# Kernel tuning notes

Measured on AMD Instinct MI355X. Metric: run time of the kernel, lower is better.

The kernel has to match this reference:

```python
import jax, jax.numpy as jnp
import numpy as np

V = 96103   # pegasus-xsum vocab
D = 1024    # d_model
H = 16      # heads
DH = D // H
F = 4096    # ffn
L = 2       # enc and dec layers (reduced from 16 for the reference)
S = 512     # source length
T = 80      # max_length
B = 4       # batch of sources
NS = 5      # num_return_sequences
BN = B * NS # decode streams
TOPK = 100
EOS = 1
MINLEN = 7
EMB_SCALE = float(np.sqrt(D))


def ln(x):
    m = jnp.mean(x, -1, keepdims=True)
    v = jnp.mean((x - m) ** 2, -1, keepdims=True)
    return (x - m) * jax.lax.rsqrt(v + 1e-5)


def setup_inputs() -> dict:
    key = jax.random.key(0)
    ks = jax.random.split(key, 16)
    g = lambda k, s: (jax.random.normal(k, s) * 0.02).astype(jnp.float32)
    return {
        "ids": jax.random.randint(ks[0], (B, S), 0, 96000).astype(jnp.int32),
        "mask": jnp.ones((B, S), jnp.int32),
        "E": g(ks[1], (V, D)),
        "pos_e": g(ks[2], (S, D)),
        "pos_d": g(ks[3], (T, D)),
        "enc_attn_in": g(ks[4], (L, D, 3 * D)),
        "enc_attn_out": g(ks[5], (L, D, D)),
        "enc_ffn1": g(ks[6], (L, D, F)),
        "enc_ffn2": g(ks[7], (L, F, D)),
        "dec_sa_in": g(ks[8], (L, D, 3 * D)),
        "dec_sa_out": g(ks[9], (L, D, D)),
        "dec_ca_q": g(ks[10], (L, D, D)),
        "dec_ca_kv": g(ks[11], (L, D, 2 * D)),
        "dec_ca_out": g(ks[12], (L, D, D)),
        "dec_ffn1": g(ks[13], (L, D, F)),
        "dec_ffn2": g(ks[14], (L, F, D)),
    }


def _generate(ids, mask, E, pos_e, pos_d, enc_attn_in, enc_attn_out, enc_ffn1,
              enc_ffn2, dec_sa_in, dec_sa_out, dec_ca_q, dec_ca_kv, dec_ca_out,
              dec_ffn1, dec_ffn2):
    inv = 1.0 / float(np.sqrt(DH))
    # ---------------- encoder ----------------
    x = E[ids] * EMB_SCALE + pos_e[None]                       # [B,S,D]
    bias = (1.0 - mask.astype(jnp.float32))[:, None, None, :] * -1e9  # [B,1,1,S]
    for l in range(L):
        h = ln(x)
        qkv = h @ enc_attn_in[l]
        q = qkv[..., :D].reshape(B, S, H, DH)
        k = qkv[..., D:2 * D].reshape(B, S, H, DH)
        v = qkv[..., 2 * D:].reshape(B, S, H, DH)
        sc = jnp.einsum('bqhd,bkhd->bhqk', q, k) * inv + bias
        a = jnp.einsum('bhqk,bkhd->bqhd', jax.nn.softmax(sc, -1), v).reshape(B, S, D)
        x = x + a @ enc_attn_out[l]
        h = ln(x)
        x = x + jax.nn.gelu(h @ enc_ffn1[l]) @ enc_ffn2[l]
    enc = ln(x)
    # expand to BN = B * num_return_sequences decode streams
    enc_r = jnp.repeat(enc, NS, axis=0)                        # [BN,S,D]
    bias_r = jnp.repeat(bias, NS, axis=0)[:, :, 0, :]          # [BN,1,S]
    # precompute cross-attn K/V per decoder layer
    ckv = jnp.einsum('bsd,lde->lbse', enc_r, dec_ca_kv)        # [L,BN,S,2D]
    cK = ckv[..., :D].reshape(L, BN, S, H, DH)
    cV = ckv[..., D:].reshape(L, BN, S, H, DH)

    key_base = jax.random.key(1234)
    cache_k0 = jnp.zeros((L, BN, T, H, DH), jnp.float32)
    cache_v0 = jnp.zeros((L, BN, T, H, DH), jnp.float32)

    def step(carry, t):
        ck, cv, prev = carry
        x = E[prev] * EMB_SCALE + pos_d[t]                     # [BN,D]
        for l in range(L):
            h = ln(x)
            qkv = h @ dec_sa_in[l]
            q = qkv[:, :D].reshape(BN, H, DH)
            k = qkv[:, D:2 * D].reshape(BN, H, DH)
            v = qkv[:, 2 * D:].reshape(BN, H, DH)
            ck = ck.at[l, :, t].set(k)
            cv = cv.at[l, :, t].set(v)
            sc = jnp.einsum('bhd,bkhd->bhk', q, ck[l]) * inv
            sc = sc + jnp.where(jnp.arange(T) <= t, 0.0, -1e9)
            a = jnp.einsum('bhk,bkhd->bhd', jax.nn.softmax(sc, -1), cv[l]).reshape(BN, D)
            x = x + a @ dec_sa_out[l]
            h = ln(x)
            q2 = (h @ dec_ca_q[l]).reshape(BN, H, DH)
            sc2 = jnp.einsum('bhd,bshd->bhs', q2, cK[l]) * inv + bias_r
            a2 = jnp.einsum('bhs,bshd->bhd', jax.nn.softmax(sc2, -1), cV[l]).reshape(BN, D)
            x = x + a2 @ dec_ca_out[l]
            h = ln(x)
            x = x + jax.nn.gelu(h @ dec_ffn1[l]) @ dec_ffn2[l]
        x = ln(x)
        logits = x @ E.T                                       # [BN,V]
        forbid = (t < MINLEN - 1) & (jnp.arange(V) == EOS)     # min_length: block EOS
        logits = jnp.where(forbid, -1e9, logits)
        topv, topi = jax.lax.top_k(logits, TOPK)               # top_k=100 sampling
        sel = jax.random.categorical(jax.random.fold_in(key_base, t), topv)
        tok = jnp.take_along_axis(topi, sel[:, None], 1)[:, 0]
        lp = jnp.take_along_axis(jax.nn.log_softmax(logits, -1), tok[:, None], 1)[:, 0]
        return (ck, cv, tok), (tok, lp)

    init = (cache_k0, cache_v0, jnp.zeros((BN,), jnp.int32))  # start token = pad(0)
    _, (toks, lps) = jax.lax.scan(step, init, jnp.arange(T))
    return toks.T, lps.T                                       # [BN,T] each


def reference(ids, mask, E, pos_e, pos_d, enc_attn_in, enc_attn_out, enc_ffn1,
              enc_ffn2, dec_sa_in, dec_sa_out, dec_ca_q, dec_ca_kv, dec_ca_out,
              dec_ffn1, dec_ffn2):
    toks, _ = _generate(ids, mask, E, pos_e, pos_d, enc_attn_in, enc_attn_out,
                        enc_ffn1, enc_ffn2, dec_sa_in, dec_sa_out, dec_ca_q,
                        dec_ca_kv, dec_ca_out, dec_ffn1, dec_ffn2)
    # matches the torch module: [batch, num_seq, max_len] token ids
    return toks.reshape(B, NS, T)
```

## Files before the change

### kernel.cpp

```cpp
#include <hip/hip_runtime.h>
#include <cstdint>
#include <cstddef>

#define DEV __device__ __forceinline__

constexpr int V  = 96103;
constexpr int D  = 1024;
constexpr int H  = 16;
constexpr int DH = 64;
constexpr int F  = 4096;
constexpr int NL = 2;
constexpr int S  = 512;
constexpr int T  = 80;
constexpr int B  = 4;
constexpr int NS = 5;
constexpr int BN = 20;
constexpr int KTOP = 100;
constexpr int EOS = 1;


DEV float gelu_f(float x) {
  float x3 = x * x * x;
  float inner = 0.7978845608028654f * (x + 0.044715f * x3);
  float tt = tanhf(inner);
  return x * (0.5f * (1.0f + tt));
}

DEV void tf2x32(unsigned k0, unsigned k1, unsigned& x0, unsigned& x1) {
  unsigned ks2 = k0 ^ k1 ^ 0x1BD11BDAu;
#define TFR(rr) { x0 += x1; x1 = (x1 << rr) | (x1 >> (32 - rr)); x1 ^= x0; }
  x0 += k0; x1 += k1;
  TFR(13) TFR(15) TFR(26) TFR(6)
  x0 += k1;  x1 += ks2 + 1u;
  TFR(17) TFR(29) TFR(16) TFR(24)
  x0 += ks2; x1 += k0 + 2u;
  TFR(13) TFR(15) TFR(26) TFR(6)
  x0 += k0;  x1 += k1 + 3u;
  TFR(17) TFR(29) TFR(16) TFR(24)
  x0 += k1;  x1 += ks2 + 4u;
  TFR(13) TFR(15) TFR(26) TFR(6)
  x0 += ks2; x1 += k0 + 5u;
#undef TFR
}

DEV unsigned long long sort_key(float v, unsigned idx) {
  unsigned bb = __float_as_uint(v);
  bb = (bb & 0x80000000u) ? ~bb : (bb | 0x80000000u);
  return ((unsigned long long)bb << 32) | (unsigned long long)(0xFFFFFFFFu - idx);
}

template<int NWAVE>
DEV void ln_to_lds(const float* __restrict__ x, float* xs, int tid) {
  int w = tid >> 6, lane = tid & 63;
  for (int m = w; m < BN; m += NWAVE) {
    float4 v[4];
    float sum = 0.0f;
#pragma unroll
    for (int j = 0; j < 4; ++j) {
      v[j] = *(const float4*)(x + m * D + j * 256 + lane * 4);
      sum += v[j].x + v[j].y + v[j].z + v[j].w;
    }
#pragma unroll
    for (int o = 32; o > 0; o >>= 1) sum += __shfl_xor(sum, o);
    float mean = sum * (1.0f / 1024.0f);
    float vs = 0.0f;
#pragma unroll
    for (int j = 0; j < 4; ++j) {
      float a = v[j].x - mean, b = v[j].y - mean, c = v[j].z - mean, d = v[j].w - mean;
      vs += a * a + b * b + c * c + d * d;
    }
#pragma unroll
    for (int o = 32; o > 0; o >>= 1) vs += __shfl_xor(vs, o);
    float rsig = 1.0f / sqrtf(vs * (1.0f / 1024.0f) + 1e-5f);
#pragma unroll
    for (int j = 0; j < 4; ++j) {
      float4 ov;
      ov.x = (v[j].x - mean) * rsig; ov.y = (v[j].y - mean) * rsig;
      ov.z = (v[j].z - mean) * rsig; ov.w = (v[j].w - mean) * rsig;
      *(float4*)(xs + m * D + j * 256 + lane * 4) = ov;
    }
  }
}


__global__ __launch_bounds__(256) void embed_enc(const int* __restrict__ ids,
                                                 const float* __restrict__ E,
                                                 const float* __restrict__ pos_e,
                                                 float* __restrict__ xe) {
  int row = blockIdx.x;
  int id = ids[row];
  const float* er = E + (size_t)id * D;
  const float* pr = pos_e + (size_t)(row % S) * D;
  float* xr = xe + (size_t)row * D;
  for (int j = threadIdx.x; j < D; j += 256)
    xr[j] = er[j] * 32.0f + pr[j];
}

__global__ __launch_bounds__(256) void embed_dec(const float* __restrict__ E,
                                                 const float* __restrict__ pos_d,
                                                 const int* __restrict__ toks,
                                                 float* __restrict__ xd, int t) {
  int bn = blockIdx.x;
  int prev = (t == 0) ? 0 : toks[bn * T + (t - 1)];
  const float* er = E + (size_t)prev * D;
  const float* pr = pos_d + (size_t)t * D;
  float* xr = xd + (size_t)bn * D;
  for (int j = threadIdx.x; j < D; j += 256)
    xr[j] = er[j] * 32.0f + pr[j];
}


__global__ __launch_bounds__(256) void ln_kernel(const float* __restrict__ x,
                                                 float* __restrict__ y) {
  __shared__ float red[256];
  __shared__ float sv[2];
  int tid = threadIdx.x;
  const float* xr = x + (size_t)blockIdx.x * D;
  float4 v = *(const float4*)(xr + tid * 4);
  red[tid] = v.x + v.y + v.z + v.w;
  __syncthreads();
  for (int k = 128; k > 0; k >>= 1) { if (tid < k) red[tid] += red[tid + k]; __syncthreads(); }
  if (tid == 0) sv[0] = red[0] * (1.0f / 1024.0f);
  __syncthreads();
  float m = sv[0];
  float dx = v.x - m, dy = v.y - m, dz = v.z - m, dw = v.w - m;
  red[tid] = dx * dx + dy * dy + dz * dz + dw * dw;
  __syncthreads();
  for (int k = 128; k > 0; k >>= 1) { if (tid < k) red[tid] += red[tid + k]; __syncthreads(); }
  if (tid == 0) sv[1] = 1.0f / sqrtf(red[0] * (1.0f / 1024.0f) + 1e-5f);
  __syncthreads();
  float r = sv[1];
  float* yr = y + (size_t)blockIdx.x * D;
  float4 o; o.x = dx * r; o.y = dy * r; o.z = dz * r; o.w = dw * r;
  *(float4*)(yr + tid * 4) = o;
}


template<int EPI>
__global__ __launch_bounds__(256) void gemm128(const float* __restrict__ A,
                                               const float* __restrict__ W,
                                               const float* X, float* C,
                                               int Kd, int Nd) {
  __shared__ __align__(16) float As[8][128];
  __shared__ __align__(16) float Bs[8][128];
  int tid = threadIdx.x;
  int n0 = blockIdx.x * 128, m0 = blockIdx.y * 128;
  int tx = tid & 15, ty = tid >> 4;
  int ar = tid >> 1, ac = (tid & 1) * 4;
  int br = tid >> 5, bc = (tid & 31) * 4;
  float acc[8][8] = {};
  for (int k0 = 0; k0 < Kd; k0 += 8) {
    float4 av = *(const float4*)(A + (size_t)(m0 + ar) * Kd + k0 + ac);
    float4 wv = *(const float4*)(W + (size_t)(k0 + br) * Nd + n0 + bc);
    __syncthreads();
    As[ac + 0][ar] = av.x; As[ac + 1][ar] = av.y;
    As[ac + 2][ar] = av.z; As[ac + 3][ar] = av.w;
    *(float4*)&Bs[br][bc] = wv;
    __syncthreads();
#pragma unroll
    for (int k = 0; k < 8; ++k) {
      float a8[8], b8[8];
      *(float4*)&a8[0] = *(const float4*)&As[k][ty * 8];
      *(float4*)&a8[4] = *(const float4*)&As[k][ty * 8 + 4];
      *(float4*)&b8[0] = *(const float4*)&Bs[k][tx * 8];
      *(float4*)&b8[4] = *(const float4*)&Bs[k][tx * 8 + 4];
#pragma unroll
      for (int i = 0; i < 8; ++i)
#pragma unroll
        for (int j = 0; j < 8; ++j)
          acc[i][j] = fmaf(a8[i], b8[j], acc[i][j]);
    }
  }
#pragma unroll
  for (int i = 0; i < 8; ++i) {
    int m = m0 + ty * 8 + i;
#pragma unroll
    for (int j = 0; j < 8; ++j) {
      int n = n0 + tx * 8 + j;
      float r = acc[i][j];
      size_t off = (size_t)m * Nd + n;
      if (EPI == 1) r = X[off] + r;
      if (EPI == 2) r = gelu_f(r);
      C[off] = r;
    }
  }
}


__global__ __launch_bounds__(256) void enc_attn(const float* __restrict__ qkv,
                                                const int* __restrict__ mask,
                                                float* __restrict__ ab) {
  __shared__ __align__(16) float qv[64];
  __shared__ float sc[512];
  __shared__ float red[256];
  __shared__ float sv[2];
  int tid = threadIdx.x;
  int q = blockIdx.x % S;
  int h = (blockIdx.x / S) % H;
  int b = blockIdx.x / (S * H);
  const float* qrow = qkv + (size_t)(b * S + q) * (3 * D) + h * 64;
  if (tid < 64) qv[tid] = qrow[tid];
  __syncthreads();
  float lmax = -INFINITY;
  for (int k = tid; k < S; k += 256) {
    const float* kr = qkv + (size_t)(b * S + k) * (3 * D) + D + h * 64;
    float dot = 0.0f;
#pragma unroll
    for (int d4 = 0; d4 < 16; ++d4) {
      float4 kk = *(const float4*)(kr + d4 * 4);
      float4 qq = *(const float4*)(qv + d4 * 4);
      dot += qq.x * kk.x + qq.y * kk.y + qq.z * kk.z + qq.w * kk.w;
    }
    float bias = (1.0f - (float)mask[b * S + k]) * -1e9f;
    float val = dot * 0.125f + bias;
    sc[k] = val;
    lmax = fmaxf(lmax, val);
  }
  red[tid] = lmax; __syncthreads();
  for (int k = 128; k > 0; k >>= 1) { if (tid < k) red[tid] = fmaxf(red[tid], red[tid + k]); __syncthreads(); }
  if (tid == 0) sv[0] = red[0];
  __syncthreads();
  float mx = sv[0];
  float lsum = 0.0f;
  for (int k = tid; k < S; k += 256) { float e = expf(sc[k] - mx); sc[k] = e; lsum += e; }
  red[tid] = lsum; __syncthreads();
  for (int k = 128; k > 0; k >>= 1) { if (tid < k) red[tid] += red[tid + k]; __syncthreads(); }
  if (tid == 0) sv[1] = red[0];
  __syncthreads();
  float den = sv[1];
  for (int k = tid; k < S; k += 256) sc[k] = sc[k] / den;
  __syncthreads();
  int d = tid & 63, c = tid >> 6;
  const float* vb = qkv + (size_t)(b * S) * (3 * D) + 2 * D + h * 64 + d;
  float part = 0.0f;
  for (int k = c * 128; k < c * 128 + 128; ++k)
    part = fmaf(sc[k], vb[(size_t)k * (3 * D)], part);
  red[tid] = part; __syncthreads();
  if (tid < 64) {
    float o = red[tid] + red[tid + 64] + red[tid + 128] + red[tid + 192];
    ab[(size_t)(b * S + q) * D + h * 64 + tid] = o;
  }
}


template<int CT, int EPI, bool KV, bool LNIN>
__global__ __launch_bounds__(512) void dec_gemm(const float* __restrict__ x,
                                                const float* __restrict__ W,
                                                const float* Xres, float* Cout,
                                                float* __restrict__ cacheK,
                                                float* __restrict__ cacheV,
                                                int Kd, int Nd, int t, int l) {
  constexpr int KSP = 512 / CT;
  __shared__ float red[CT * 20 * (KSP + 1)];
  __shared__ float redw[CT * (KSP + 1)];
  __shared__ float sab[40];
  int tid = threadIdx.x;
  if constexpr (LNIN) {
    int w = tid >> 6, lane = tid & 63;
    for (int m = w; m < BN; m += 8) {
      const float* xr = x + (size_t)m * 1024 + lane * 16;
      float4 v[4];
      float sum = 0.0f;
#pragma unroll
      for (int j = 0; j < 4; ++j) {
        v[j] = *(const float4*)(xr + j * 4);
        sum += v[j].x + v[j].y + v[j].z + v[j].w;
      }
#pragma unroll
      for (int o = 32; o > 0; o >>= 1) sum += __shfl_xor(sum, o);
      float mean = sum * (1.0f / 1024.0f);
      float vs = 0.0f;
#pragma unroll
      for (int j = 0; j < 4; ++j) {
        float a = v[j].x - mean, b = v[j].y - mean, c2 = v[j].z - mean, d = v[j].w - mean;
        vs += a * a + b * b + c2 * c2 + d * d;
      }
#pragma unroll
      for (int o = 32; o > 0; o >>= 1) vs += __shfl_xor(vs, o);
      float rstd = 1.0f / sqrtf(vs * (1.0f / 1024.0f) + 1e-5f);
      if (lane == 0) { sab[m] = rstd; sab[20 + m] = -mean * rstd; }
    }
    __syncthreads();
  }
  int c = tid % CT, ks = tid / CT;
  int klen = Kd / KSP;
  const float* Wp = W + (size_t)(ks * klen) * Nd + blockIdx.x * CT + c;
  float acc[20] = {};
  float accw = 0.0f;
  for (int kk = 0; kk < klen; kk += 8) {
    float wv[8];
#pragma unroll
    for (int u = 0; u < 8; ++u) wv[u] = Wp[(size_t)u * Nd];
    Wp += (size_t)8 * Nd;
    if constexpr (LNIN) {
      accw += wv[0] + wv[1] + wv[2] + wv[3] + wv[4] + wv[5] + wv[6] + wv[7];
    }
    int kb = ks * klen + kk;
#pragma unroll
    for (int m = 0; m < 20; ++m) {
      float4 x0 = *(const float4*)(x + (size_t)m * Kd + kb);
      float4 x1 = *(const float4*)(x + (size_t)m * Kd + kb + 4);
      float a = acc[m];
      a = fmaf(x0.x, wv[0], a); a = fmaf(x0.y, wv[1], a);
      a = fmaf(x0.z, wv[2], a); a = fmaf(x0.w, wv[3], a);
      a = fmaf(x1.x, wv[4], a); a = fmaf(x1.y, wv[5], a);
      a = fmaf(x1.z, wv[6], a); a = fmaf(x1.w, wv[7], a);
      acc[m] = a;
    }
  }
#pragma unroll
  for (int m = 0; m < 20; ++m) red[(c * 20 + m) * (KSP + 1) + ks] = acc[m];
  if constexpr (LNIN) redw[c * (KSP + 1) + ks] = accw;
  __syncthreads();
  if (tid < CT * 20) {
    int cc = tid % CT, m = tid / CT;
    const float* rp = red + (cc * 20 + m) * (KSP + 1);
    float s = 0.0f;
#pragma unroll
    for (int k2 = 0; k2 < KSP; ++k2) s += rp[k2];
    if constexpr (LNIN) {
      const float* rw = redw + cc * (KSP + 1);
      float sw = 0.0f;
#pragma unroll
      for (int k2 = 0; k2 < KSP; ++k2) sw += rw[k2];
      s = sab[m] * s + sab[20 + m] * sw;
    }
    int ng = blockIdx.x * CT + cc;
    if constexpr (KV) {
      if (ng < D) {
        Cout[(size_t)m * Nd + ng] = s;
      } else if (ng < 2 * D) {
        cacheK[(((size_t)l * BN + m) * T + t) * D + (ng - D)] = s;
      } else {
        cacheV[(((size_t)l * BN + m) * T + t) * D + (ng - 2 * D)] = s;
      }
    } else {
      size_t off = (size_t)m * Nd + ng;
      if (EPI == 1) s = Xres[off] + s;
      if (EPI == 2) s = gelu_f(s);
      Cout[off] = s;
    }
  }
}


__global__ __launch_bounds__(128) void dec_self_attn(const float* __restrict__ qkvd,
                                                     const float* __restrict__ cacheK,
                                                     const float* __restrict__ cacheV,
                                                     float* __restrict__ ad, int t, int l) {
  __shared__ __align__(16) float qv[64];
  __shared__ float sc[96];
  __shared__ float sv[2];
  int tid = threadIdx.x;
  int bn = blockIdx.x >> 4;
  int h = blockIdx.x & 15;
  int n = t + 1;
  if (tid < 64) qv[tid] = qkvd[(size_t)bn * (3 * D) + h * 64 + tid];
  __syncthreads();
  if (tid < n) {
    const float* kr = cacheK + (((size_t)l * BN + bn) * T + tid) * D + h * 64;
    float dot = 0.0f;
#pragma unroll
    for (int d4 = 0; d4 < 16; ++d4) {
      float4 kk = *(const float4*)(kr + d4 * 4);
      float4 qq = *(const float4*)(qv + d4 * 4);
      dot += qq.x * kk.x + qq.y * kk.y + qq.z * kk.z + qq.w * kk.w;
    }
    sc[tid] = dot * 0.125f;
  }
  __syncthreads();
  if (tid == 0) {
    float mx = -INFINITY;
    for (int k = 0; k < n; ++k) mx = fmaxf(mx, sc[k]);
    sv[0] = mx;
  }
  __syncthreads();
  if (tid < n) sc[tid] = expf(sc[tid] - sv[0]);
  __syncthreads();
  if (tid == 0) {
    float s = 0.0f;
    for (int k = 0; k < n; ++k) s += sc[k];
    sv[1] = s;
  }
  __syncthreads();
  if (tid < n) sc[tid] = sc[tid] / sv[1];
  __syncthreads();
  if (tid < 64) {
    const float* vb = cacheV + ((size_t)l * BN + bn) * T * D + h * 64 + tid;
    float o = 0.0f;
    for (int k = 0; k < n; ++k) o = fmaf(sc[k], vb[(size_t)k * D], o);
    ad[(size_t)bn * D + h * 64 + tid] = o;
  }
}


__global__ __launch_bounds__(256) void dec_cross_attn(const float* __restrict__ q2,
                                                      const float* __restrict__ cKV,
                                                      const int* __restrict__ mask,
                                                      float* __restrict__ ad, int l) {
  __shared__ __align__(16) float qv[64];
  __shared__ float sc[512];
  __shared__ float red[256];
  __shared__ float sv[2];
  int tid = threadIdx.x;
  int bn = blockIdx.x >> 4;
  int h = blockIdx.x & 15;
  int b = bn / NS;
  const float* base = cKV + ((size_t)l * B + b) * S * (2 * D);
  if (tid < 64) qv[tid] = q2[(size_t)bn * D + h * 64 + tid];
  __syncthreads();
  float lmax = -INFINITY;
  for (int s = tid; s < S; s += 256) {
    const float* kr = base + (size_t)s * (2 * D) + h * 64;
    float dot = 0.0f;
#pragma unroll
    for (int d4 = 0; d4 < 16; ++d4) {
      float4 kk = *(const float4*)(kr + d4 * 4);
      float4 qq = *(const float4*)(qv + d4 * 4);
      dot += qq.x * kk.x + qq.y * kk.y + qq.z * kk.z + qq.w * kk.w;
    }
    float bias = (1.0f - (float)mask[b * S + s]) * -1e9f;
    float val = dot * 0.125f + bias;
    sc[s] = val;
    lmax = fmaxf(lmax, val);
  }
  red[tid] = lmax; __syncthreads();
  for (int k = 128; k > 0; k >>= 1) { if (tid < k) red[tid] = fmaxf(red[tid], red[tid + k]); __syncthreads(); }
  if (tid == 0) sv[0] = red[0];
  __syncthreads();
  float mx = sv[0];
  float lsum = 0.0f;
  for (int s = tid; s < S; s += 256) { float e = expf(sc[s] - mx); sc[s] = e; lsum += e; }
  red[tid] = lsum; __syncthreads();
  for (int k = 128; k > 0; k >>= 1) { if (tid < k) red[tid] += red[tid + k]; __syncthreads(); }
  if (tid == 0) sv[1] = red[0];
  __syncthreads();
  float den = sv[1];
  for (int s = tid; s < S; s += 256) sc[s] = sc[s] / den;
  __syncthreads();
  int d = tid & 63, c = tid >> 6;
  const float* vb = base + D + h * 64 + d;
  float part = 0.0f;
  for (int s = c * 128; s < c * 128 + 128; ++s)
    part = fmaf(sc[s], vb[(size_t)s * (2 * D)], part);
  red[tid] = part; __syncthreads();
  if (tid < 64) {
    float o = red[tid] + red[tid + 64] + red[tid + 128] + red[tid + 192];
    ad[(size_t)bn * D + h * 64 + tid] = o;
  }
}


__global__ __launch_bounds__(256) void logits_ln(const float* __restrict__ xd,
                                                 const float* __restrict__ E,
                                                 float* __restrict__ logits) {
  __shared__ float xs[20 * 1024];
  int tid = threadIdx.x;
  ln_to_lds<4>(xd, xs, tid);
  __syncthreads();
  int w = tid >> 6, l = tid & 63;
  int mh = (w >> 1) * 10;
  int ns = w & 1;
  int nb = blockIdx.x * 384 + ns * 192 + l;
  int n1 = nb + 64, n2 = nb + 128;
  const float* e0 = E + (size_t)(nb < V ? nb : V - 1) * D;
  const float* e1 = E + (size_t)(n1 < V ? n1 : V - 1) * D;
  const float* e2 = E + (size_t)(n2 < V ? n2 : V - 1) * D;
  const float* xb = xs + mh * 1024;
  float acc[10][3] = {};
  for (int k = 0; k < 1024; k += 4) {
    float4 ea = *(const float4*)(e0 + k);
    float4 eb = *(const float4*)(e1 + k);
    float4 ec = *(const float4*)(e2 + k);
#pragma unroll
    for (int m = 0; m < 10; ++m) {
      const float4 xv = *(const float4*)(xb + m * 1024 + k);
      float a0 = acc[m][0], a1 = acc[m][1], a2 = acc[m][2];
      a0 = fmaf(xv.x, ea.x, a0); a0 = fmaf(xv.y, ea.y, a0);
      a0 = fmaf(xv.z, ea.z, a0); a0 = fmaf(xv.w, ea.w, a0);
      a1 = fmaf(xv.x, eb.x, a1); a1 = fmaf(xv.y, eb.y, a1);
      a1 = fmaf(xv.z, eb.z, a1); a1 = fmaf(xv.w, eb.w, a1);
      a2 = fmaf(xv.x, ec.x, a2); a2 = fmaf(xv.y, ec.y, a2);
      a2 = fmaf(xv.z, ec.z, a2); a2 = fmaf(xv.w, ec.w, a2);
      acc[m][0] = a0; acc[m][1] = a1; acc[m][2] = a2;
    }
  }
#pragma unroll
  for (int m = 0; m < 10; ++m) {
    if (nb < V) logits[(size_t)(mh + m) * V + nb] = acc[m][0];
    if (n1 < V) logits[(size_t)(mh + m) * V + n1] = acc[m][1];
    if (n2 < V) logits[(size_t)(mh + m) * V + n2] = acc[m][2];
  }
}


__global__ __launch_bounds__(256) void topk_sample(const float* __restrict__ logits,
                                                   int* __restrict__ toks, int t) {
  __shared__ unsigned long long keys[2048];
  __shared__ float svals[128];
  __shared__ unsigned sidx[128];
  int tid = threadIdx.x;
  int bn = blockIdx.x;
  const float* row = logits + (size_t)bn * V;

  float tv[8]; unsigned ti[8];
#pragma unroll
  for (int j = 0; j < 8; ++j) { tv[j] = -INFINITY; ti[j] = 0xFFFFFFFFu; }

  for (int i = tid; i < V; i += 256) {
    float v = row[i];
    if (t < 6 && i == EOS) v = -1e9f;
    if (v > tv[7]) {
      tv[7] = v; ti[7] = (unsigned)i;
#pragma unroll
      for (int j = 7; j > 0; --j) {
        if (tv[j] > tv[j - 1]) {
          float a = tv[j]; tv[j] = tv[j - 1]; tv[j - 1] = a;
          unsigned bi = ti[j]; ti[j] = ti[j - 1]; ti[j - 1] = bi;
        }
      }
    }
  }
#pragma unroll
  for (int j = 0; j < 8; ++j) keys[tid * 8 + j] = ~sort_key(tv[j], ti[j]);
  __syncthreads();

  for (int ksz = 2; ksz <= 2048; ksz <<= 1) {
    for (int jj = ksz >> 1; jj > 0; jj >>= 1) {
      for (int i = tid; i < 2048; i += 256) {
        int ixj = i ^ jj;
        if (ixj > i) {
          unsigned long long a = keys[i], b2 = keys[ixj];
          bool up = ((i & ksz) == 0);
          if ((a > b2) == up) { keys[i] = b2; keys[ixj] = a; }
        }
      }
      __syncthreads();
    }
  }

  if (tid < KTOP) {
    unsigned long long kk = ~keys[tid];
    unsigned sb = (unsigned)(kk >> 32);
    unsigned idx = 0xFFFFFFFFu - (unsigned)(kk & 0xFFFFFFFFull);
    unsigned fb = (sb & 0x80000000u) ? (sb ^ 0x80000000u) : ~sb;
    float v = __uint_as_float(fb);
    unsigned a0 = 0u, a1 = (unsigned)t;
    tf2x32(0u, 1234u, a0, a1);
    unsigned c0 = 0u, c1 = (unsigned)(bn * KTOP + tid);
    tf2x32(a0, a1, c0, c1);
    unsigned bits = c0 ^ c1;
    float f = __uint_as_float((bits >> 9) | 0x3f800000u) - 1.0f;
    float u = fmaxf(f, 1.17549435e-38f);
    float g = -logf(-logf(u));
    svals[tid] = v + g;
    sidx[tid] = idx;
  }
  __syncthreads();
  if (tid == 0) {
    int best = 0; float bv = svals[0];
    for (int j = 1; j < KTOP; ++j) { if (svals[j] > bv) { bv = svals[j]; best = j; } }
    toks[bn * T + t] = (int)sidx[best];
  }
}


extern "C" void kernel_launch(void* const* d_in, const int* in_sizes, int n_in,
                              void* d_out, int out_size, void* d_ws, size_t ws_size,
                              hipStream_t stream) {
  (void)in_sizes; (void)n_in; (void)out_size; (void)ws_size;

  const int*   ids   = (const int*)d_in[0];
  const int*   maskp = (const int*)d_in[1];
  const float* E     = (const float*)d_in[2];
  const float* pos_e = (const float*)d_in[3];
  const float* pos_d = (const float*)d_in[4];
  const float* eai   = (const float*)d_in[5];
  const float* eao   = (const float*)d_in[6];
  const float* ef1   = (const float*)d_in[7];
  const float* ef2   = (const float*)d_in[8];
  const float* dsi   = (const float*)d_in[9];
  const float* dso   = (const float*)d_in[10];
  const float* dcq   = (const float*)d_in[11];
  const float* dckv  = (const float*)d_in[12];
  const float* dco   = (const float*)d_in[13];
  const float* df1   = (const float*)d_in[14];
  const float* df2   = (const float*)d_in[15];

  float* ws = (float*)d_ws;
  size_t o = 0;
  auto alloc = [&](size_t n) { size_t r = o; o += (n + 63) & ~(size_t)63; return r; };
  float* cKV    = ws + alloc((size_t)NL * B * S * 2 * D);
  float* cacheK = ws + alloc((size_t)NL * BN * T * D);
  float* cacheV = ws + alloc((size_t)NL * BN * T * D);
  float* xe     = ws + alloc((size_t)B * S * D);
  float* he     = ws + alloc((size_t)B * S * D);
  float* qkvb   = ws + alloc((size_t)B * S * 3 * D);
  float* ab     = ws + alloc((size_t)B * S * D);
  float* ffb    = ws + alloc((size_t)B * S * F);
  float* xd      = qkvb;
  float* q2      = xd + BN * D;
  float* ad      = q2 + BN * D;
  float* qkvd    = ad + BN * D;
  float* ffd     = qkvd + BN * 3 * D;
  float* logitsb = ffd + BN * F;
  int* toks = (int*)d_out;

  embed_enc<<<B * S, 256, 0, stream>>>(ids, E, pos_e, xe);
  for (int l = 0; l < NL; ++l) {
    ln_kernel<<<B * S, 256, 0, stream>>>(xe, he);
    gemm128<0><<<dim3(3 * D / 128, B * S / 128), 256, 0, stream>>>(
        he, eai + (size_t)l * D * 3 * D, nullptr, qkvb, D, 3 * D);
    enc_attn<<<B * H * S, 256, 0, stream>>>(qkvb, maskp, ab);
    gemm128<1><<<dim3(D / 128, B * S / 128), 256, 0, stream>>>(
        ab, eao + (size_t)l * D * D, xe, xe, D, D);
    ln_kernel<<<B * S, 256, 0, stream>>>(xe, he);
    gemm128<2><<<dim3(F / 128, B * S / 128), 256, 0, stream>>>(
        he, ef1 + (size_t)l * D * F, nullptr, ffb, D, F);
    gemm128<1><<<dim3(D / 128, B * S / 128), 256, 0, stream>>>(
        ffb, ef2 + (size_t)l * F * D, xe, xe, F, D);
  }
  ln_kernel<<<B * S, 256, 0, stream>>>(xe, he);
  for (int l = 0; l < NL; ++l) {
    gemm128<0><<<dim3(2 * D / 128, B * S / 128), 256, 0, stream>>>(
        he, dckv + (size_t)l * D * 2 * D, nullptr,
        cKV + (size_t)l * B * S * 2 * D, D, 2 * D);
  }

  for (int t = 0; t < T; ++t) {
    embed_dec<<<BN, 256, 0, stream>>>(E, pos_d, toks, xd, t);
    for (int l = 0; l < NL; ++l) {
      dec_gemm<16, 0, true, true><<<3 * D / 16, 512, 0, stream>>>(
          xd, dsi + (size_t)l * D * 3 * D, nullptr, qkvd, cacheK, cacheV,
          D, 3 * D, t, l);
      dec_self_attn<<<BN * H, 128, 0, stream>>>(qkvd, cacheK, cacheV, ad, t, l);
      dec_gemm<8, 1, false, false><<<D / 8, 512, 0, stream>>>(
          ad, dso + (size_t)l * D * D, xd, xd, nullptr, nullptr, D, D, 0, 0);
      dec_gemm<8, 0, false, true><<<D / 8, 512, 0, stream>>>(
          xd, dcq + (size_t)l * D * D, nullptr, q2, nullptr, nullptr, D, D, 0, 0);
      dec_cross_attn<<<BN * H, 256, 0, stream>>>(q2, cKV, maskp, ad, l);
      dec_gemm<8, 1, false, false><<<D / 8, 512, 0, stream>>>(
          ad, dco + (size_t)l * D * D, xd, xd, nullptr, nullptr, D, D, 0, 0);
      dec_gemm<16, 2, false, true><<<F / 16, 512, 0, stream>>>(
          xd, df1 + (size_t)l * D * F, nullptr, ffd, nullptr, nullptr, D, F, 0, 0);
      dec_gemm<8, 1, false, false><<<D / 8, 512, 0, stream>>>(
          ffd, df2 + (size_t)l * F * D, xd, xd, nullptr, nullptr, F, D, 0, 0);
    }
    logits_ln<<<(V + 383) / 384, 256, 0, stream>>>(xd, E, logitsb);
    topk_sample<<<BN, 256, 0, stream>>>(logitsb, toks, t);
  }
}
```

Before: 63.65 ms.

## Fuse decode loop into one persistent kernel with grid-wide barriers

Replaces the per-step chain of about 19 kernel launches over 80 decode steps with a single persistent 256-block kernel that runs every phase as a device function, separated by a custom global barrier built on flags and atomics. Embedding of the next token is folded into the top-k phase, and the logits LayerNorm is applied algebraically, using per-row mean and rstd times the dot product plus the embedding row sum, instead of normalizing into shared memory. The goal is to remove launch overhead and inter-kernel gaps. In exchange the GEMM phases use fewer blocks (grids capped at 256), the logits phase loops over 251 tiles with fewer rows per wave, and correctness depends on all blocks being co-resident.

```diff
diff --git a/kernel.cpp b/kernel.cpp
--- a/kernel.cpp
+++ b/kernel.cpp
@@ -17,6 +17,10 @@
 constexpr int BN = 20;
 constexpr int KTOP = 100;
 constexpr int EOS = 1;
+
+constexpr int NBLK = 256;
+constexpr int NTHR = 512;
+constexpr int LTILES = (V + 383) / 384;
 
 
 DEV float gelu_f(float x) {
@@ -49,37 +53,28 @@
   return ((unsigned long long)bb << 32) | (unsigned long long)(0xFFFFFFFFu - idx);
 }
 
-template<int NWAVE>
-DEV void ln_to_lds(const float* __restrict__ x, float* xs, int tid) {
-  int w = tid >> 6, lane = tid & 63;
-  for (int m = w; m < BN; m += NWAVE) {
-    float4 v[4];
-    float sum = 0.0f;
-#pragma unroll
-    for (int j = 0; j < 4; ++j) {
-      v[j] = *(const float4*)(x + m * D + j * 256 + lane * 4);
-      sum += v[j].x + v[j].y + v[j].z + v[j].w;
-    }
-#pragma unroll
-    for (int o = 32; o > 0; o >>= 1) sum += __shfl_xor(sum, o);
-    float mean = sum * (1.0f / 1024.0f);
-    float vs = 0.0f;
-#pragma unroll
-    for (int j = 0; j < 4; ++j) {
-      float a = v[j].x - mean, b = v[j].y - mean, c = v[j].z - mean, d = v[j].w - mean;
-      vs += a * a + b * b + c * c + d * d;
-    }
-#pragma unroll
-    for (int o = 32; o > 0; o >>= 1) vs += __shfl_xor(vs, o);
-    float rsig = 1.0f / sqrtf(vs * (1.0f / 1024.0f) + 1e-5f);
-#pragma unroll
-    for (int j = 0; j < 4; ++j) {
-      float4 ov;
-      ov.x = (v[j].x - mean) * rsig; ov.y = (v[j].y - mean) * rsig;
-      ov.z = (v[j].z - mean) * rsig; ov.w = (v[j].w - mean) * rsig;
-      *(float4*)(xs + m * D + j * 256 + lane * 4) = ov;
-    }
-  }
+DEV void gbar(unsigned* __restrict__ flags, unsigned* __restrict__ rel, unsigned gen) {
+  __syncthreads();
+  __threadfence();
+  if (threadIdx.x == 0)
+    __hip_atomic_store(&flags[blockIdx.x], gen, __ATOMIC_RELEASE, __HIP_MEMORY_SCOPE_AGENT);
+  if (blockIdx.x == 0) {
+    int i = threadIdx.x;
+    if (i < NBLK) {
+      while (__hip_atomic_load(&flags[i], __ATOMIC_RELAXED, __HIP_MEMORY_SCOPE_AGENT) < gen)
+        __builtin_amdgcn_s_sleep(1);
+    }
+    __syncthreads();
+    if (threadIdx.x == 0)
+      __hip_atomic_store(rel, gen, __ATOMIC_RELEASE, __HIP_MEMORY_SCOPE_AGENT);
+  }
+  if (threadIdx.x == 0) {
+    while (__hip_atomic_load(rel, __ATOMIC_RELAXED, __HIP_MEMORY_SCOPE_AGENT) < gen)
+      __builtin_amdgcn_s_sleep(1);
+    (void)__hip_atomic_load(rel, __ATOMIC_ACQUIRE, __HIP_MEMORY_SCOPE_AGENT);
+  }
+  __syncthreads();
+  __threadfence();
 }
 
 
@@ -96,20 +91,6 @@
     xr[j] = er[j] * 32.0f + pr[j];
 }
 
-__global__ __launch_bounds__(256) void embed_dec(const float* __restrict__ E,
-                                                 const float* __restrict__ pos_d,
-                                                 const int* __restrict__ toks,
-                                                 float* __restrict__ xd, int t) {
-  int bn = blockIdx.x;
-  int prev = (t == 0) ? 0 : toks[bn * T + (t - 1)];
-  const float* er = E + (size_t)prev * D;
-  const float* pr = pos_d + (size_t)t * D;
-  float* xr = xd + (size_t)bn * D;
-  for (int j = threadIdx.x; j < D; j += 256)
-    xr[j] = er[j] * 32.0f + pr[j];
-}
-
-
 __global__ __launch_bounds__(256) void ln_kernel(const float* __restrict__ x,
                                                  float* __restrict__ y) {
   __shared__ float red[256];
@@ -134,7 +115,6 @@
   float4 o; o.x = dx * r; o.y = dy * r; o.z = dz * r; o.w = dw * r;
   *(float4*)(yr + tid * 4) = o;
 }
-
 
 template<int EPI>
 __global__ __launch_bounds__(256) void gemm128(const float* __restrict__ A,
@@ -186,7 +166,6 @@
   }
 }
 
-
 __global__ __launch_bounds__(256) void enc_attn(const float* __restrict__ qkv,
                                                 const int* __restrict__ mask,
                                                 float* __restrict__ ab) {
@@ -244,17 +223,15 @@
 
 
 template<int CT, int EPI, bool KV, bool LNIN>
-__global__ __launch_bounds__(512) void dec_gemm(const float* __restrict__ x,
-                                                const float* __restrict__ W,
-                                                const float* Xres, float* Cout,
-                                                float* __restrict__ cacheK,
-                                                float* __restrict__ cacheV,
-                                                int Kd, int Nd, int t, int l) {
-  constexpr int KSP = 512 / CT;
-  __shared__ float red[CT * 20 * (KSP + 1)];
-  __shared__ float redw[CT * (KSP + 1)];
-  __shared__ float sab[40];
-  int tid = threadIdx.x;
+DEV void p_gemm(const float* __restrict__ x, const float* __restrict__ W,
+                const float* Xres, float* Cout,
+                float* __restrict__ cacheK, float* __restrict__ cacheV,
+                int Kd, int Nd, int t, int l, char* smemc, int bid, int tid) {
+  constexpr int KSP = NTHR / CT;
+  if (bid * CT >= Nd) return;
+  float* red  = (float*)smemc;
+  float* redw = red + CT * 20 * (KSP + 1);
+  float* sab  = redw + CT * (KSP + 1);
   if constexpr (LNIN) {
     int w = tid >> 6, lane = tid & 63;
     for (int m = w; m < BN; m += 8) {
@@ -284,7 +261,7 @@
   }
   int c = tid % CT, ks = tid / CT;
   int klen = Kd / KSP;
-  const float* Wp = W + (size_t)(ks * klen) * Nd + blockIdx.x * CT + c;
+  const float* Wp = W + (size_t)(ks * klen) * Nd + bid * CT + c;
   float acc[20] = {};
   float accw = 0.0f;
   for (int kk = 0; kk < klen; kk += 8) {
@@ -292,9 +269,8 @@
 #pragma unroll
     for (int u = 0; u < 8; ++u) wv[u] = Wp[(size_t)u * Nd];
     Wp += (size_t)8 * Nd;
-    if constexpr (LNIN) {
+    if constexpr (LNIN)
       accw += wv[0] + wv[1] + wv[2] + wv[3] + wv[4] + wv[5] + wv[6] + wv[7];
-    }
     int kb = ks * klen + kk;
 #pragma unroll
     for (int m = 0; m < 20; ++m) {
@@ -316,16 +292,14 @@
     int cc = tid % CT, m = tid / CT;
     const float* rp = red + (cc * 20 + m) * (KSP + 1);
     float s = 0.0f;
-#pragma unroll
     for (int k2 = 0; k2 < KSP; ++k2) s += rp[k2];
     if constexpr (LNIN) {
       const float* rw = redw + cc * (KSP + 1);
       float sw = 0.0f;
-#pragma unroll
       for (int k2 = 0; k2 < KSP; ++k2) sw += rw[k2];
       s = sab[m] * s + sab[20 + m] * sw;
     }
-    int ng = blockIdx.x * CT + cc;
+    int ng = bid * CT + cc;
     if constexpr (KV) {
       if (ng < D) {
         Cout[(size_t)m * Nd + ng] = s;
@@ -343,138 +317,170 @@
   }
 }
 
-
-__global__ __launch_bounds__(128) void dec_self_attn(const float* __restrict__ qkvd,
-                                                     const float* __restrict__ cacheK,
-                                                     const float* __restrict__ cacheV,
-                                                     float* __restrict__ ad, int t, int l) {
-  __shared__ __align__(16) float qv[64];
-  __shared__ float sc[96];
-  __shared__ float sv[2];
-  int tid = threadIdx.x;
-  int bn = blockIdx.x >> 4;
-  int h = blockIdx.x & 15;
+DEV void p_selfattn(const float* __restrict__ qkvd,
+                    const float* __restrict__ cacheK, const float* __restrict__ cacheV,
+                    float* __restrict__ ad, int t, int l, char* smemc, int bid, int tid) {
+  float* qv  = (float*)smemc;
+  float* sc  = qv + 64;
+  float* sv  = sc + 96;
+  float* red = sv + 2;
   int n = t + 1;
-  if (tid < 64) qv[tid] = qkvd[(size_t)bn * (3 * D) + h * 64 + tid];
-  __syncthreads();
-  if (tid < n) {
-    const float* kr = cacheK + (((size_t)l * BN + bn) * T + tid) * D + h * 64;
-    float dot = 0.0f;
-#pragma unroll
-    for (int d4 = 0; d4 < 16; ++d4) {
-      float4 kk = *(const float4*)(kr + d4 * 4);
-      float4 qq = *(const float4*)(qv + d4 * 4);
-      dot += qq.x * kk.x + qq.y * kk.y + qq.z * kk.z + qq.w * kk.w;
-    }
-    sc[tid] = dot * 0.125f;
-  }
-  __syncthreads();
-  if (tid == 0) {
-    float mx = -INFINITY;
-    for (int k = 0; k < n; ++k) mx = fmaxf(mx, sc[k]);
-    sv[0] = mx;
-  }
-  __syncthreads();
-  if (tid < n) sc[tid] = expf(sc[tid] - sv[0]);
-  __syncthreads();
-  if (tid == 0) {
-    float s = 0.0f;
-    for (int k = 0; k < n; ++k) s += sc[k];
-    sv[1] = s;
-  }
-  __syncthreads();
-  if (tid < n) sc[tid] = sc[tid] / sv[1];
-  __syncthreads();
-  if (tid < 64) {
-    const float* vb = cacheV + ((size_t)l * BN + bn) * T * D + h * 64 + tid;
+  for (int u = bid; u < BN * H; u += NBLK) {
+    int bn = u >> 4, h = u & 15;
+    __syncthreads();
+    if (tid < 64) qv[tid] = qkvd[(size_t)bn * (3 * D) + h * 64 + tid];
+    __syncthreads();
+    if (tid < n) {
+      const float* kr = cacheK + (((size_t)l * BN + bn) * T + tid) * D + h * 64;
+      float dot = 0.0f;
+#pragma unroll
+      for (int d4 = 0; d4 < 16; ++d4) {
+        float4 kk = *(const float4*)(kr + d4 * 4);
+        float4 qq = *(const float4*)(qv + d4 * 4);
+        dot += qq.x * kk.x + qq.y * kk.y + qq.z * kk.z + qq.w * kk.w;
+      }
+      sc[tid] = dot * 0.125f;
+    }
+    __syncthreads();
+    if (tid == 0) {
+      float mx = -INFINITY;
+      for (int k = 0; k < n; ++k) mx = fmaxf(mx, sc[k]);
+      sv[0] = mx;
+    }
+    __syncthreads();
+    if (tid < n) sc[tid] = expf(sc[tid] - sv[0]);
+    __syncthreads();
+    if (tid == 0) {
+      float s = 0.0f;
+      for (int k = 0; k < n; ++k) s += sc[k];
+      sv[1] = s;
+    }
+    __syncthreads();
+    if (tid < n) sc[tid] = sc[tid] / sv[1];
+    __syncthreads();
+    int d = tid & 63, c = tid >> 6;
+    const float* vb = cacheV + ((size_t)l * BN + bn) * T * D + h * 64 + d;
     float o = 0.0f;
-    for (int k = 0; k < n; ++k) o = fmaf(sc[k], vb[(size_t)k * D], o);
-    ad[(size_t)bn * D + h * 64 + tid] = o;
-  }
-}
-
-
-__global__ __launch_bounds__(256) void dec_cross_attn(const float* __restrict__ q2,
-                                                      const float* __restrict__ cKV,
-                                                      const int* __restrict__ mask,
-                                                      float* __restrict__ ad, int l) {
-  __shared__ __align__(16) float qv[64];
-  __shared__ float sc[512];
-  __shared__ float red[256];
-  __shared__ float sv[2];
-  int tid = threadIdx.x;
-  int bn = blockIdx.x >> 4;
-  int h = blockIdx.x & 15;
-  int b = bn / NS;
-  const float* base = cKV + ((size_t)l * B + b) * S * (2 * D);
-  if (tid < 64) qv[tid] = q2[(size_t)bn * D + h * 64 + tid];
-  __syncthreads();
-  float lmax = -INFINITY;
-  for (int s = tid; s < S; s += 256) {
-    const float* kr = base + (size_t)s * (2 * D) + h * 64;
-    float dot = 0.0f;
-#pragma unroll
-    for (int d4 = 0; d4 < 16; ++d4) {
-      float4 kk = *(const float4*)(kr + d4 * 4);
-      float4 qq = *(const float4*)(qv + d4 * 4);
-      dot += qq.x * kk.x + qq.y * kk.y + qq.z * kk.z + qq.w * kk.w;
-    }
-    float bias = (1.0f - (float)mask[b * S + s]) * -1e9f;
-    float val = dot * 0.125f + bias;
-    sc[s] = val;
-    lmax = fmaxf(lmax, val);
-  }
-  red[tid] = lmax; __syncthreads();
-  for (int k = 128; k > 0; k >>= 1) { if (tid < k) red[tid] = fmaxf(red[tid], red[tid + k]); __syncthreads(); }
-  if (tid == 0) sv[0] = red[0];
-  __syncthreads();
-  float mx = sv[0];
-  float lsum = 0.0f;
-  for (int s = tid; s < S; s += 256) { float e = expf(sc[s] - mx); sc[s] = e; lsum += e; }
-  red[tid] = lsum; __syncthreads();
-  for (int k = 128; k > 0; k >>= 1) { if (tid < k) red[tid] += red[tid + k]; __syncthreads(); }
-  if (tid == 0) sv[1] = red[0];
-  __syncthreads();
-  float den = sv[1];
-  for (int s = tid; s < S; s += 256) sc[s] = sc[s] / den;
-  __syncthreads();
-  int d = tid & 63, c = tid >> 6;
-  const float* vb = base + D + h * 64 + d;
-  float part = 0.0f;
-  for (int s = c * 128; s < c * 128 + 128; ++s)
-    part = fmaf(sc[s], vb[(size_t)s * (2 * D)], part);
-  red[tid] = part; __syncthreads();
-  if (tid < 64) {
-    float o = red[tid] + red[tid + 64] + red[tid + 128] + red[tid + 192];
-    ad[(size_t)bn * D + h * 64 + tid] = o;
-  }
-}
-
-
-__global__ __launch_bounds__(256) void logits_ln(const float* __restrict__ xd,
-                                                 const float* __restrict__ E,
-                                                 float* __restrict__ logits) {
-  __shared__ float xs[20 * 1024];
-  int tid = threadIdx.x;
-  ln_to_lds<4>(xd, xs, tid);
-  __syncthreads();
-  int w = tid >> 6, l = tid & 63;
-  int mh = (w >> 1) * 10;
-  int ns = w & 1;
-  int nb = blockIdx.x * 384 + ns * 192 + l;
-  int n1 = nb + 64, n2 = nb + 128;
-  const float* e0 = E + (size_t)(nb < V ? nb : V - 1) * D;
+    for (int k = c; k < n; k += 8) o = fmaf(sc[k], vb[(size_t)k * D], o);
+    red[c * 64 + d] = o;
+    __syncthreads();
+    if (tid < 64) {
+      float s = 0.0f;
+#pragma unroll
+      for (int g = 0; g < 8; ++g) s += red[g * 64 + tid];
+      ad[(size_t)bn * D + h * 64 + tid] = s;
+    }
+  }
+}
+
+DEV void p_crossattn(const float* __restrict__ q2, const float* __restrict__ cKVl,
+                     const int* __restrict__ mask, float* __restrict__ ad,
+                     char* smemc, int bid, int tid) {
+  float* qv  = (float*)smemc;
+  float* sc  = qv + 64;
+  float* red = sc + 512;
+  float* sv  = red + 512;
+  for (int u = bid; u < BN * H; u += NBLK) {
+    int bn = u >> 4, h = u & 15, b = bn / NS;
+    const float* base = cKVl + (size_t)b * S * (2 * D);
+    __syncthreads();
+    if (tid < 64) qv[tid] = q2[(size_t)bn * D + h * 64 + tid];
+    __syncthreads();
+    {
+      const float* kr = base + (size_t)tid * (2 * D) + h * 64;
+      float dot = 0.0f;
+#pragma unroll
+      for (int d4 = 0; d4 < 16; ++d4) {
+        float4 kk = *(const float4*)(kr + d4 * 4);
+        float4 qq = *(const float4*)(qv + d4 * 4);
+        dot += qq.x * kk.x + qq.y * kk.y + qq.z * kk.z + qq.w * kk.w;
+      }
+      float bias = (1.0f - (float)mask[b * S + tid]) * -1e9f;
+      float val = dot * 0.125f + bias;
+      sc[tid] = val;
+      red[tid] = val;
+    }
+    __syncthreads();
+    for (int k = 256; k > 0; k >>= 1) { if (tid < k) red[tid] = fmaxf(red[tid], red[tid + k]); __syncthreads(); }
+    if (tid == 0) sv[0] = red[0];
+    __syncthreads();
+    float e = expf(sc[tid] - sv[0]);
+    sc[tid] = e;
+    red[tid] = e;
+    __syncthreads();
+    for (int k = 256; k > 0; k >>= 1) { if (tid < k) red[tid] += red[tid + k]; __syncthreads(); }
+    if (tid == 0) sv[1] = red[0];
+    __syncthreads();
+    sc[tid] = sc[tid] / sv[1];
+    __syncthreads();
+    int d = tid & 63, c = tid >> 6;
+    const float* vb = base + D + h * 64 + d;
+    float part = 0.0f;
+    for (int s2 = c * 64; s2 < c * 64 + 64; ++s2)
+      part = fmaf(sc[s2], vb[(size_t)s2 * (2 * D)], part);
+    red[c * 64 + d] = part;
+    __syncthreads();
+    if (tid < 64) {
+      float s = 0.0f;
+#pragma unroll
+      for (int g = 0; g < 8; ++g) s += red[g * 64 + tid];
+      ad[(size_t)bn * D + h * 64 + tid] = s;
+    }
+  }
+}
+
+DEV void p_logits(const float* __restrict__ xd, const float* __restrict__ E,
+                  float* __restrict__ logits, char* smemc, int bid, int tid) {
+  if (bid >= LTILES) return;
+  float* sab = (float*)smemc;
+  {
+    int w = tid >> 6, lane = tid & 63;
+    for (int m = w; m < BN; m += 8) {
+      const float* xr = xd + (size_t)m * 1024 + lane * 16;
+      float4 v[4];
+      float sum = 0.0f;
+#pragma unroll
+      for (int j = 0; j < 4; ++j) {
+        v[j] = *(const float4*)(xr + j * 4);
+        sum += v[j].x + v[j].y + v[j].z + v[j].w;
+      }
+#pragma unroll
+      for (int o = 32; o > 0; o >>= 1) sum += __shfl_xor(sum, o);
+      float mean = sum * (1.0f / 1024.0f);
+      float vs = 0.0f;
+#pragma unroll
+      for (int j = 0; j < 4; ++j) {
+        float a = v[j].x - mean, b = v[j].y - mean, c2 = v[j].z - mean, d = v[j].w - mean;
+        vs += a * a + b * b + c2 * c2 + d * d;
+      }
+#pragma unroll
+      for (int o = 32; o > 0; o >>= 1) vs += __shfl_xor(vs, o);
+      float rstd = 1.0f / sqrtf(vs * (1.0f / 1024.0f) + 1e-5f);
+      if (lane == 0) { sab[m] = rstd; sab[20 + m] = -mean * rstd; }
+    }
+    __syncthreads();
+  }
+  int w = tid >> 6, lane = tid & 63;
+  int mh = (w >> 1) * 5;
+  int cs = w & 1;
+  int n0 = bid * 384 + cs * 192 + lane;
+  int n1 = n0 + 64, n2 = n0 + 128;
+  const float* e0 = E + (size_t)(n0 < V ? n0 : V - 1) * D;
   const float* e1 = E + (size_t)(n1 < V ? n1 : V - 1) * D;
   const float* e2 = E + (size_t)(n2 < V ? n2 : V - 1) * D;
-  const float* xb = xs + mh * 1024;
-  float acc[10][3] = {};
+  const float* xb = xd + (size_t)mh * D;
+  float acc[5][3] = {};
+  float se0 = 0.0f, se1 = 0.0f, se2 = 0.0f;
   for (int k = 0; k < 1024; k += 4) {
     float4 ea = *(const float4*)(e0 + k);
     float4 eb = *(const float4*)(e1 + k);
     float4 ec = *(const float4*)(e2 + k);
-#pragma unroll
-    for (int m = 0; m < 10; ++m) {
-      const float4 xv = *(const float4*)(xb + m * 1024 + k);
+    se0 += ea.x + ea.y + ea.z + ea.w;
+    se1 += eb.x + eb.y + eb.z + eb.w;
+    se2 += ec.x + ec.y + ec.z + ec.w;
+#pragma unroll
+    for (int m = 0; m < 5; ++m) {
+      float4 xv = *(const float4*)(xb + (size_t)m * D + k);
       float a0 = acc[m][0], a1 = acc[m][1], a2 = acc[m][2];
       a0 = fmaf(xv.x, ea.x, a0); a0 = fmaf(xv.y, ea.y, a0);
       a0 = fmaf(xv.z, ea.z, a0); a0 = fmaf(xv.w, ea.w, a0);
@@ -486,28 +492,30 @@
     }
   }
 #pragma unroll
-  for (int m = 0; m < 10; ++m) {
-    if (nb < V) logits[(size_t)(mh + m) * V + nb] = acc[m][0];
-    if (n1 < V) logits[(size_t)(mh + m) * V + n1] = acc[m][1];
-    if (n2 < V) logits[(size_t)(mh + m) * V + n2] = acc[m][2];
-  }
-}
-
-
-__global__ __launch_bounds__(256) void topk_sample(const float* __restrict__ logits,
-                                                   int* __restrict__ toks, int t) {
-  __shared__ unsigned long long keys[2048];
-  __shared__ float svals[128];
-  __shared__ unsigned sidx[128];
-  int tid = threadIdx.x;
-  int bn = blockIdx.x;
+  for (int m = 0; m < 5; ++m) {
+    int row = mh + m;
+    float a = sab[row], b = sab[20 + row];
+    if (n0 < V) logits[(size_t)row * V + n0] = a * acc[m][0] + b * se0;
+    if (n1 < V) logits[(size_t)row * V + n1] = a * acc[m][1] + b * se1;
+    if (n2 < V) logits[(size_t)row * V + n2] = a * acc[m][2] + b * se2;
+  }
+}
+
+DEV void p_topk(const float* __restrict__ logits, int* __restrict__ toks,
+                const float* __restrict__ E, const float* __restrict__ pos_d,
+                float* __restrict__ xd, int t, char* smemc, int bid, int tid) {
+  if (bid >= BN) return;
+  unsigned long long* keys = (unsigned long long*)smemc;
+  float*    svals = (float*)(smemc + 32768);
+  unsigned* sidx  = (unsigned*)(smemc + 32768 + 512);
+  int*      stok  = (int*)(smemc + 32768 + 1024);
+  int bn = bid;
   const float* row = logits + (size_t)bn * V;
 
   float tv[8]; unsigned ti[8];
 #pragma unroll
   for (int j = 0; j < 8; ++j) { tv[j] = -INFINITY; ti[j] = 0xFFFFFFFFu; }
-
-  for (int i = tid; i < V; i += 256) {
+  for (int i = tid; i < V; i += NTHR) {
     float v = row[i];
     if (t < 6 && i == EOS) v = -1e9f;
     if (v > tv[7]) {
@@ -525,9 +533,9 @@
   for (int j = 0; j < 8; ++j) keys[tid * 8 + j] = ~sort_key(tv[j], ti[j]);
   __syncthreads();
 
-  for (int ksz = 2; ksz <= 2048; ksz <<= 1) {
+  for (int ksz = 2; ksz <= 4096; ksz <<= 1) {
     for (int jj = ksz >> 1; jj > 0; jj >>= 1) {
-      for (int i = tid; i < 2048; i += 256) {
+      for (int i = tid; i < 4096; i += NTHR) {
         int ixj = i ^ jj;
         if (ixj > i) {
           unsigned long long a = keys[i], b2 = keys[ixj];
@@ -560,7 +568,71 @@
   if (tid == 0) {
     int best = 0; float bv = svals[0];
     for (int j = 1; j < KTOP; ++j) { if (svals[j] > bv) { bv = svals[j]; best = j; } }
-    toks[bn * T + t] = (int)sidx[best];
+    int tok = (int)sidx[best];
+    toks[bn * T + t] = tok;
+    *stok = tok;
+  }
+  __syncthreads();
+  if (t + 1 < T) {
+    int tok = *stok;
+    const float* er = E + (size_t)tok * D;
+    const float* pr = pos_d + (size_t)(t + 1) * D;
+    for (int j = tid; j < D; j += NTHR)
+      xd[(size_t)bn * D + j] = er[j] * 32.0f + pr[j];
+  }
+}
+
+
+__global__ __launch_bounds__(NTHR, 2) void decode_persist(
+    const float* __restrict__ E, const float* __restrict__ pos_d,
+    const int* __restrict__ maskp,
+    const float* __restrict__ dsi, const float* __restrict__ dso,
+    const float* __restrict__ dcq, const float* __restrict__ dco,
+    const float* __restrict__ df1, const float* __restrict__ df2,
+    const float* __restrict__ cKV,
+    float* cacheK, float* cacheV,
+    float* xd, float* q2, float* ad, float* qkvd, float* ffd, float* logitsb,
+    int* toks, unsigned* gflags, unsigned* grel) {
+  __shared__ __align__(16) char smem[46080];
+  int bid = blockIdx.x, tid = threadIdx.x;
+  unsigned gen = 0;
+
+  if (bid < BN) {
+    float* xr = xd + (size_t)bid * D;
+    for (int j = tid; j < D; j += NTHR)
+      xr[j] = E[j] * 32.0f + pos_d[j];
+  }
+  gbar(gflags, grel, ++gen);
+
+  for (int t = 0; t < T; ++t) {
+    for (int l = 0; l < NL; ++l) {
+      p_gemm<16, 0, true, true>(xd, dsi + (size_t)l * D * 3 * D, nullptr, qkvd,
+                                cacheK, cacheV, D, 3 * D, t, l, smem, bid, tid);
+      gbar(gflags, grel, ++gen);
+      p_selfattn(qkvd, cacheK, cacheV, ad, t, l, smem, bid, tid);
+      gbar(gflags, grel, ++gen);
+      p_gemm<4, 1, false, false>(ad, dso + (size_t)l * D * D, xd, xd,
+                                 nullptr, nullptr, D, D, 0, 0, smem, bid, tid);
+      gbar(gflags, grel, ++gen);
+      p_gemm<4, 0, false, true>(xd, dcq + (size_t)l * D * D, nullptr, q2,
+                                nullptr, nullptr, D, D, 0, 0, smem, bid, tid);
+      gbar(gflags, grel, ++gen);
+      p_crossattn(q2, cKV + (size_t)l * B * S * 2 * D, maskp, ad, smem, bid, tid);
+      gbar(gflags, grel, ++gen);
+      p_gemm<4, 1, false, false>(ad, dco + (size_t)l * D * D, xd, xd,
+                                 nullptr, nullptr, D, D, 0, 0, smem, bid, tid);
+      gbar(gflags, grel, ++gen);
+      p_gemm<16, 2, false, true>(xd, df1 + (size_t)l * D * F, nullptr, ffd,
+                                 nullptr, nullptr, D, F, 0, 0, smem, bid, tid);
+      gbar(gflags, grel, ++gen);
+      p_gemm<4, 1, false, false>(ffd, df2 + (size_t)l * F * D, xd, xd,
+                                 nullptr, nullptr, F, D, 0, 0, smem, bid, tid);
+      gbar(gflags, grel, ++gen);
+    }
+    p_logits(xd, E, logitsb, smem, bid, tid);
+    gbar(gflags, grel, ++gen);
+    p_topk(logitsb, toks, E, pos_d, xd, t, smem, bid, tid);
+    gbar(gflags, grel, ++gen);
   }
 }
 
@@ -587,7 +659,9 @@
   const float* df1   = (const float*)d_in[14];
   const float* df2   = (const float*)d_in[15];
 
-  float* ws = (float*)d_ws;
+  unsigned* gflags = (unsigned*)d_ws;
+  unsigned* grel   = gflags + NBLK;
+  float* ws = (float*)((char*)d_ws + 4096);
   size_t o = 0;
   auto alloc = [&](size_t n) { size_t r = o; o += (n + 63) & ~(size_t)63; return r; };
   float* cKV    = ws + alloc((size_t)NL * B * S * 2 * D);
@@ -606,6 +680,8 @@
   float* logitsb = ffd + BN * F;
   int* toks = (int*)d_out;
 
+  hipMemsetAsync(d_ws, 0, 4096, stream);
+
   embed_enc<<<B * S, 256, 0, stream>>>(ids, E, pos_e, xe);
   for (int l = 0; l < NL; ++l) {
     ln_kernel<<<B * S, 256, 0, stream>>>(xe, he);
@@ -627,26 +703,7 @@
         cKV + (size_t)l * B * S * 2 * D, D, 2 * D);
   }
 
-  for (int t = 0; t < T; ++t) {
-    embed_dec<<<BN, 256, 0, stream>>>(E, pos_d, toks, xd, t);
-    for (int l = 0; l < NL; ++l) {
-      dec_gemm<16, 0, true, true><<<3 * D / 16, 512, 0, stream>>>(
-          xd, dsi + (size_t)l * D * 3 * D, nullptr, qkvd, cacheK, cacheV,
-          D, 3 * D, t, l);
-      dec_self_attn<<<BN * H, 128, 0, stream>>>(qkvd, cacheK, cacheV, ad, t, l);
-      dec_gemm<8, 1, false, false><<<D / 8, 512, 0, stream>>>(
-          ad, dso + (size_t)l * D * D, xd, xd, nullptr, nullptr, D, D, 0, 0);
-      dec_gemm<8, 0, false, true><<<D / 8, 512, 0, stream>>>(
-          xd, dcq + (size_t)l * D * D, nullptr, q2, nullptr, nullptr, D, D, 0, 0);
-      dec_cross_attn<<<BN * H, 256, 0, stream>>>(q2, cKV, maskp, ad, l);
-      dec_gemm<8, 1, false, false><<<D / 8, 512, 0, stream>>>(
-          ad, dco + (size_t)l * D * D, xd, xd, nullptr, nullptr, D, D, 0, 0);
-      dec_gemm<16, 2, false, true><<<F / 16, 512, 0, stream>>>(
-          xd, df1 + (size_t)l * D * F, nullptr, ffd, nullptr, nullptr, D, F, 0, 0);
-      dec_gemm<8, 1, false, false><<<D / 8, 512, 0, stream>>>(
-          ffd, df2 + (size_t)l * F * D, xd, xd, nullptr, nullptr, F, D, 0, 0);
-    }
-    logits_ln<<<(V + 383) / 384, 256, 0, stream>>>(xd, E, logitsb);
-    topk_sample<<<BN, 256, 0, stream>>>(logitsb, toks, t);
-  }
-}
+  decode_persist<<<NBLK, NTHR, 0, stream>>>(
+      E, pos_d, maskp, dsi, dso, dcq, dco, df1, df2, cKV,
+      cacheK, cacheV, xd, q2, ad, qkvd, ffd, logitsb, toks, gflags, grel);
+}
```

Result: slower. 185.1 ms (+190.8%).
